# Optimization experiments

Measured on AMD Instinct MI355X. Metric: run time of the kernel, lower is better.

## Reference

```python
import jax, jax.numpy as jnp
import numpy as np

KS = 2        # kernel_size
DIL = 1       # dilation
FILTERS = 512
Z_DIM = 128
B, C, T = 8, 512, 4096
TZ = T + 2 * (KS - 1)


def _conv1d(x, w, b):
    # x: (B, L, Cin), w: (ks, Cin, Cout) -> VALID conv, channels-last (keras Conv1D)
    y = jax.lax.conv_general_dilated(x, w, window_strides=(1,), padding='VALID',
                                     dimension_numbers=('NWC', 'WIO', 'NWC'))
    return y + b


def _adaptor(z, w1, b1, w2, b2):
    return _conv1d(jax.nn.relu(_conv1d(z, w1, b1)), w2, b2)


def setup_inputs() -> dict:
    key = jax.random.key(0)
    ks = jax.random.split(key, 10)
    lim = np.sqrt(6.0 / FILTERS)
    u = lambda k, shp: jax.random.uniform(k, shp, jnp.float32, -lim, lim)
    return {
        'x': jax.random.normal(ks[0], (B, C, T), jnp.float32),
        'z': jax.random.normal(ks[1], (B, TZ, Z_DIM), jnp.float32),
        'ww1': u(ks[2], (KS, Z_DIM, FILTERS)), 'wb1': jnp.zeros((FILTERS,), jnp.float32),
        'ww2': u(ks[3], (KS, FILTERS, FILTERS)), 'wb2': jnp.zeros((FILTERS,), jnp.float32),
        'bw1': u(ks[4], (KS, Z_DIM, FILTERS)), 'bb1': jnp.zeros((FILTERS,), jnp.float32),
        'bw2': u(ks[5], (KS, FILTERS, FILTERS)), 'bb2': jnp.zeros((FILTERS,), jnp.float32),
    }


def reference(x, z, ww1, wb1, ww2, wb2, bw1, bb1, bw2, bb2):
    m = x.shape[1]
    t = x.shape[2]
    pad = DIL * (KS - 1)
    xp = jnp.pad(x, ((0, 0), (0, 0), (0, pad)))
    end = t + pad
    # im2col-style unfold: (B, C*KS, T)
    xu = jnp.concatenate([xp[:, :, pad - i * DIL: end - i * DIL] for i in range(KS)], axis=1)
    weights = _adaptor(z, ww1, wb1, ww2, wb2)   # (B, T, F)
    bias = _adaptor(z, bw1, bb1, bw2, bb2)      # (B, T, F)
    y = jnp.matmul(xu, weights)                 # (B, C*KS, F)
    return y[:, :m, :] + bias[:, :m, :]
```

## Files before the change

kernel.cpp:

```cpp
#include <hip/hip_runtime.h>

typedef short short8 __attribute__((ext_vector_type(8)));
typedef float float4v __attribute__((ext_vector_type(4)));
typedef __attribute__((address_space(1))) const unsigned int gu32;
typedef __attribute__((address_space(3))) unsigned int lu32;

__device__ __forceinline__ unsigned short f2bf(float f) {
  unsigned int u = __builtin_bit_cast(unsigned int, f);
  u += 0x7FFFu + ((u >> 16) & 1u);
  return (unsigned short)(u >> 16);
}
__device__ __forceinline__ float bf2f(unsigned short s) {
  return __builtin_bit_cast(float, (unsigned int)s << 16);
}

__global__ __launch_bounds__(256) void prep_w(
    const float* __restrict__ ww1, const float* __restrict__ ww2,
    const float* __restrict__ bw1, const float* __restrict__ bw2,
    const float* __restrict__ z,
    unsigned short* __restrict__ w1T, unsigned short* __restrict__ w2T,
    unsigned short* __restrict__ b1T, unsigned short* __restrict__ b2T,
    unsigned short* __restrict__ zb)
{
  int i = blockIdx.x * 256 + threadIdx.x;
  if (i < 131072) {
    int n = i & 511, k = i >> 9;
    w1T[n * 256 + k] = f2bf(ww1[i]);
  } else if (i < 655360) {
    int j = i - 131072; int n = j & 511, k = j >> 9;
    w2T[n * 1024 + k] = f2bf(ww2[j]);
  } else if (i < 786432) {
    int j = i - 655360; int n = j & 511, k = j >> 9;
    b1T[n * 256 + k] = f2bf(bw1[j]);
  } else if (i < 1310720) {
    int j = i - 786432; int n = j & 511, k = j >> 9;
    b2T[n * 1024 + k] = f2bf(bw2[j]);
  } else {
    int j = i - 1310720;
    zb[j] = f2bf(z[j]);
  }
}

template<int BM, int BN, bool RELU, bool OBF16, bool TRANS, bool SPLITK, int NH,
         bool ROWPACK, bool DBUF>
__device__ __forceinline__ void gemm_core(
    int bx, int by, int bz, int nzTot, unsigned short* smem,
    const unsigned short* __restrict__ A,
    const unsigned short* __restrict__ A2,
    const unsigned short* __restrict__ Bt,
    const float* __restrict__ biasv,
    void* __restrict__ outp,
    void* __restrict__ outp2,
    int M, int Kchunk, int RPB, int EXTRA, int BSCALE,
    int nHalf, int bRowMask,
    long long bStrideB, long long outBatchStride, int outLd)
{
  constexpr int WM = BM / 2, WN = BN / 2;
  constexpr int NI = WM / 16, NJ = WN / 16;
  constexpr int AI = BM / 64;
  constexpr int BI = BN / 64;
  constexpr int SA1 = BM * 32, SB1 = BN * 32;
  static_assert(!DBUF || (AI + BI == 4), "vmcnt immediates assume 4 glds/stage");
  unsigned short* sB0 = smem + NH * SA1;

  const int tid  = threadIdx.x;
  const int lane = tid & 63;
  const int wave = tid >> 6;
  const int wm = wave >> 1, wn = wave & 1;
  const int lr = lane & 15, quad = lane >> 4;

  const int r0 = bx * BM;
  const int n0 = by * BN;
  const int bb = r0 / RPB;
  const int Ktot = SPLITK ? Kchunk * nzTot : Kchunk;
  const int kOff = SPLITK ? bz * Kchunk : 0;
  const long long bOffB = (long long)bb * bStrideB;
  const unsigned short* Ae = (nHalf && n0 >= nHalf) ? A2 : A;

  const int srow = lane >> 2;
  const int sg = (lane & 3) ^ (srow & 3);
  const unsigned short* gA[AI];
#pragma unroll
  for (int c = 0; c < AI; ++c) {
    int instr = c * 4 + wave;
    int row = instr * 16 + srow;
    int r = r0 + row; if (r > M - 1) r = M - 1;
    gA[c] = Ae + ((long long)r + (long long)(r / RPB) * EXTRA) * BSCALE + kOff + sg * 8;
  }
  const unsigned short* gB[BI];
#pragma unroll
  for (int c = 0; c < BI; ++c) {
    int instr = c * 4 + wave;
    int row = instr * 16 + srow;
    gB[c] = Bt + (long long)((n0 + row) & bRowMask) * Ktot + bOffB + kOff + sg * 8;
  }

  int aoff[NI], boff[NJ];
#pragma unroll
  for (int i = 0; i < NI; ++i) {
    int rr = wm * WM + i * 16 + lr;
    aoff[i] = rr * 32 + ((quad ^ (rr & 3)) * 8);
  }
#pragma unroll
  for (int j = 0; j < NJ; ++j) {
    int rr = wn * WN + j * 16 + lr;
    boff[j] = rr * 32 + ((quad ^ (rr & 3)) * 8);
  }

  float4v acc[NI][NJ];
  const float4v z4 = {0.f, 0.f, 0.f, 0.f};
#pragma unroll
  for (int i = 0; i < NI; ++i)
#pragma unroll
    for (int j = 0; j < NJ; ++j) acc[i][j] = z4;

  if (DBUF) {
    constexpr int RS = SA1 + SB1;
    const int NT = Kchunk >> 5;
    auto stg = [&](int t, int m) {
      unsigned short* rb = smem + m * RS;
      int kk = t * 32;
#pragma unroll
      for (int c = 0; c < AI; ++c)
        __builtin_amdgcn_global_load_lds((gu32*)(gA[c] + kk),
                                         (lu32*)(rb + (c * 4 + wave) * 512), 16, 0, 0);
#pragma unroll
      for (int c = 0; c < BI; ++c)
        __builtin_amdgcn_global_load_lds((gu32*)(gB[c] + kk),
                                         (lu32*)(rb + SA1 + (c * 4 + wave) * 512), 16, 0, 0);
    };
    stg(0, 0); stg(1, 1);
    int m = 0;
    for (int t = 0; t < NT; ++t) {
      if (t + 1 < NT) asm volatile("s_waitcnt vmcnt(4)" ::: "memory");
      else            asm volatile("s_waitcnt vmcnt(0)" ::: "memory");
      __builtin_amdgcn_s_barrier();
      __builtin_amdgcn_sched_barrier(0);
      int m2 = m + 2; if (m2 >= 3) m2 -= 3;
      if (t + 2 < NT) stg(t + 2, m2);
      const unsigned short* rb = smem + m * RS;
      short8 af[NI], bfr[NJ];
#pragma unroll
      for (int i = 0; i < NI; ++i) af[i] = *(const short8*)(rb + aoff[i]);
#pragma unroll
      for (int j = 0; j < NJ; ++j) bfr[j] = *(const short8*)(rb + SA1 + boff[j]);
#pragma unroll
      for (int i = 0; i < NI; ++i)
#pragma unroll
        for (int j = 0; j < NJ; ++j)
          acc[i][j] = __builtin_amdgcn_mfma_f32_16x16x32_bf16(af[i], bfr[j], acc[i][j], 0, 0, 0);
      if (++m == 3) m = 0;
    }
    __syncthreads();
  } else {
    for (int k0 = 0; k0 < Kchunk; k0 += 32 * NH) {
#pragma unroll
      for (int h = 0; h < NH; ++h) {
#pragma unroll
        for (int c = 0; c < AI; ++c)
          __builtin_amdgcn_global_load_lds((gu32*)(gA[c] + k0 + h * 32),
                                           (lu32*)(smem + (c * 4 + wave) * 512 + h * SA1), 16, 0, 0);
#pragma unroll
        for (int c = 0; c < BI; ++c)
          __builtin_amdgcn_global_load_lds((gu32*)(gB[c] + k0 + h * 32),
                                           (lu32*)(sB0 + (c * 4 + wave) * 512 + h * SB1), 16, 0, 0);
      }
      __syncthreads();
#pragma unroll
      for (int h = 0; h < NH; ++h) {
        short8 af[NI], bfr[NJ];
#pragma unroll
        for (int i = 0; i < NI; ++i) af[i] = *(const short8*)(smem + h * SA1 + aoff[i]);
#pragma unroll
        for (int j = 0; j < NJ; ++j) bfr[j] = *(const short8*)(sB0 + h * SB1 + boff[j]);
#pragma unroll
        for (int i = 0; i < NI; ++i)
#pragma unroll
          for (int j = 0; j < NJ; ++j)
            acc[i][j] = __builtin_amdgcn_mfma_f32_16x16x32_bf16(af[i], bfr[j], acc[i][j], 0, 0, 0);
      }
      __syncthreads();
    }
  }

  if (TRANS) {
    unsigned short* Ts = smem;
    const int t0l = r0 - bb * RPB;
#pragma unroll
    for (int p = 0; p < 2; ++p) {
      if (wn == p) {
#pragma unroll
        for (int j = 0; j < NJ; ++j) {
          int frl = j * 16 + lr;
          float bv = biasv[n0 + p * WN + frl];
#pragma unroll
          for (int i = 0; i < NI; ++i) {
            int tr = wm * WM + i * 16 + quad * 4;
            unsigned long long pk = 0;
#pragma unroll
            for (int g = 0; g < 4; ++g) {
              float vv = acc[i][j][g] + bv;
              if (RELU) vv = fmaxf(vv, 0.f);
              pk |= (unsigned long long)f2bf(vv) << (16 * g);
            }
            *(unsigned long long*)(Ts + frl * (BM + 8) + tr) = pk;
          }
        }
      }
      __syncthreads();
      int frl = tid >> 2, sgg = tid & 3;
      unsigned short* dst = (unsigned short*)outp + (long long)bb * outBatchStride
                          + (long long)(n0 + p * WN + frl) * outLd + t0l + sgg * (BM / 4);
      const unsigned short* srcp = Ts + frl * (BM + 8) + sgg * (BM / 4);
#pragma unroll
      for (int u = 0; u < BM / 32; ++u)
        *(uint4*)(dst + u * 8) = *(const uint4*)(srcp + u * 8);
      __syncthreads();
    }
  } else if (ROWPACK) {
    constexpr int P  = (BM > 64) ? 2 : 1;
    constexpr int RP = BM / P;
    constexpr int BNP = BN + 8;
    constexpr int TPR = 256 / RP;
    constexpr int EPT = BN / TPR;
    void* op = (SPLITK && bz) ? outp2 : outp;
    unsigned short* R = smem;
#pragma unroll
    for (int p = 0; p < P; ++p) {
      if (P == 1 || wm == p) {
#pragma unroll
        for (int j = 0; j < NJ; ++j) {
          int cc = wn * WN + j * 16 + lr;
#pragma unroll
          for (int i = 0; i < NI; ++i) {
            int rl = (P == 1 ? wm * WM : 0) + i * 16 + quad * 4;
#pragma unroll
            for (int g = 0; g < 4; ++g)
              R[(rl + g) * BNP + cc] = f2bf(acc[i][j][g]);
          }
        }
      }
      __syncthreads();
      int rloc = tid / TPR, part = tid % TPR;
      unsigned short* dstp = (unsigned short*)op
                           + (long long)(r0 + p * RP + rloc) * outLd + n0 + part * EPT;
      const unsigned short* srcp = R + rloc * BNP + part * EPT;
#pragma unroll
      for (int u = 0; u < EPT / 8; ++u)
        *(uint4*)(dstp + u * 8) = *(const uint4*)(srcp + u * 8);
      if (p + 1 < P) __syncthreads();
    }
  } else {
    void* op = (SPLITK && bz) ? outp2 : outp;
#pragma unroll
    for (int j = 0; j < NJ; ++j) {
      int n_g = n0 + wn * WN + j * 16 + lr;
      float bv = biasv ? biasv[n_g] : 0.f;
#pragma unroll
      for (int i = 0; i < NI; ++i) {
        int r_base = r0 + wm * WM + i * 16 + quad * 4;
#pragma unroll
        for (int g = 0; g < 4; ++g) {
          int r_g = r_base + g;
          if (r_g >= M) continue;
          float v = acc[i][j][g] + bv;
          if (RELU) v = fmaxf(v, 0.f);
          long long oidx = (long long)r_g * outLd + n_g;
          if (OBF16) ((unsigned short*)op)[oidx] = f2bf(v);
          else       ((float*)op)[oidx] = v;
        }
      }
    }
  }
}

template<int BM, int BN, bool RELU, bool OBF16, bool TRANS, bool SPLITK, int NH,
         bool ROWPACK, bool DBUF, bool REMAP8>
__global__ __launch_bounds__(256)
void gemm_bt(const unsigned short* __restrict__ A,
             const unsigned short* __restrict__ A2,
             const unsigned short* __restrict__ Bt,
             const float* __restrict__ biasv,
             void* __restrict__ outp,
             void* __restrict__ outp2,
             int M, int Kchunk, int RPB, int EXTRA, int BSCALE,
             int nHalf, int bRowMask,
             long long bStrideB, long long outBatchStride, int outLd)
{
  constexpr int STAGE = DBUF ? 3 * (BM * 32 + BN * 32) : NH * (BM * 32 + BN * 32);
  constexpr int REPK = TRANS ? (BN / 2) * (BM + 8)
                     : (ROWPACK ? (BM > 64 ? (BM / 2) * (BN + 8) : BM * (BN + 8)) : 0);
  constexpr int SMEMN = (REPK > STAGE) ? REPK : STAGE;
  __shared__ unsigned short smem[SMEMN];
  int bx, by, bz, nz;
  if (REMAP8) {
    int lin = blockIdx.x;
    by = lin & 7;
    int pos = lin >> 3;
    bz = pos >> 5;
    bx = pos & 31;
    nz = 2;
  } else {
    bx = blockIdx.x; by = blockIdx.y; bz = blockIdx.z; nz = gridDim.z;
  }
  gemm_core<BM, BN, RELU, OBF16, TRANS, SPLITK, NH, ROWPACK, DBUF>(
      bx, by, bz, nz, smem,
      A, A2, Bt, biasv, outp, outp2,
      M, Kchunk, RPB, EXTRA, BSCALE, nHalf, bRowMask,
      bStrideB, outBatchStride, outLd);
}

__global__ __launch_bounds__(256) void mega(
    const float* __restrict__ x,
    const unsigned short* __restrict__ zb,
    const unsigned short* __restrict__ w1T,
    const unsigned short* __restrict__ b1T,
    const float* __restrict__ wb1,
    const float* __restrict__ bb1,
    unsigned short* __restrict__ h1T,
    unsigned short* __restrict__ h1b,
    unsigned short* __restrict__ xs,
    unsigned short* __restrict__ xz,
    float* __restrict__ rs)
{
  __shared__ unsigned short smem[8704];
  int b = blockIdx.x;
  int g = (b * 1284) / 5380;
  bool isg = (((b + 1) * 1284) / 5380) > g;
  if (isg) {
    if (g < 1024) {
      gemm_core<128, 128, true, true, true, false, 1, false, false>(
          g & 255, g >> 8, 0, 1, smem,
          zb, nullptr, w1T, wb1, h1T, nullptr,
          32768, 256, 4096, 2, 128, 0, 0xFFFF, 0, 512ll * 4096, 4096);
    } else {
      int idx = g - 1024;
      gemm_core<64, 128, true, true, false, false, 1, false, false>(
          idx % 65, idx / 65, 0, 1, smem,
          zb, nullptr, b1T, bb1, h1b, nullptr,
          4104, 256, 513, 3585, 128, 0, 0xFFFF, 0, 0, 512);
    }
  } else {
    float* red = (float*)smem;
    long long r = b - g;
    const float* xr = x + r * 4096;
    int t0 = threadIdx.x * 16;
    float v[17];
    const float4* xr4 = (const float4*)(xr + t0);
#pragma unroll
    for (int q = 0; q < 4; ++q) {
      float4 f = xr4[q];
      v[q * 4] = f.x; v[q * 4 + 1] = f.y; v[q * 4 + 2] = f.z; v[q * 4 + 3] = f.w;
    }
    v[16] = (t0 + 16 < 4096) ? xr[t0 + 16] : 0.f;
    unsigned int spk[8], zpk[8];
    float sum = 0.f;
#pragma unroll
    for (int q = 0; q < 8; ++q) {
      unsigned short s0 = f2bf(v[2 * q + 1]);
      unsigned short s1 = f2bf(v[2 * q + 2]);
      sum += bf2f(s0);
      sum += bf2f(s1);
      spk[q] = (unsigned int)s0 | ((unsigned int)s1 << 16);
      unsigned short z0 = (t0 == 0 && q == 0) ? (unsigned short)0 : f2bf(v[2 * q]);
      unsigned short z1 = f2bf(v[2 * q + 1]);
      zpk[q] = (unsigned int)z0 | ((unsigned int)z1 << 16);
    }
    *(uint4*)(xs + r * 4096 + t0)     = *(uint4*)(spk);
    *(uint4*)(xs + r * 4096 + t0 + 8) = *(uint4*)(spk + 4);
    *(uint4*)(xz + r * 4096 + t0)     = *(uint4*)(zpk);
    *(uint4*)(xz + r * 4096 + t0 + 8) = *(uint4*)(zpk + 4);
#pragma unroll
    for (int off = 32; off > 0; off >>= 1) sum += __shfl_down(sum, off);
    if ((threadIdx.x & 63) == 0) red[threadIdx.x >> 6] = sum;
    __syncthreads();
    if (threadIdx.x == 0) rs[r] = red[0] + red[1] + red[2] + red[3];
  }
}

__global__ __launch_bounds__(256) void final_gemm3(
    const unsigned short* __restrict__ p0,
    const unsigned short* __restrict__ p1,
    const unsigned short* __restrict__ h1b,
    const unsigned short* __restrict__ w2T,
    const unsigned short* __restrict__ b2T,
    const float* __restrict__ rs,
    const float* __restrict__ wb2,
    const float* __restrict__ bb2,
    float* __restrict__ out)
{
  constexpr int RS = 8192;
  __shared__ unsigned short smem[3 * RS];
  const int tid = threadIdx.x;
  const int lane = tid & 63, wave = tid >> 6;
  const int wm = wave >> 1, wn = wave & 1;
  const int lr = lane & 15, quad = lane >> 4;
  const int r0 = blockIdx.x * 64, n0 = blockIdx.y * 64;

  const int srow = lane >> 2;
  const int sg = (lane & 3) ^ (srow & 3);
  const int row = wave * 16 + srow;
  const int rA = r0 + row;
  const int rB = n0 + row;
  const unsigned short* aP[3] = {
    p0 + (long long)rA * 1024 + sg * 8,
    p1 + (long long)rA * 1024 + sg * 8,
    h1b + ((long long)rA + (rA >> 9)) * 512 + sg * 8 };
  const unsigned short* bP[3] = {
    w2T + (long long)rB * 1024 + sg * 8,
    w2T + (long long)rB * 1024 + sg * 8,
    b2T + (long long)rB * 1024 + sg * 8 };

  int aoff[2], boff[2];
#pragma unroll
  for (int i = 0; i < 2; ++i) {
    int rr = wm * 32 + i * 16 + lr;
    aoff[i] = rr * 32 + ((quad ^ (rr & 3)) * 8);
    int nn = wn * 32 + i * 16 + lr;
    boff[i] = nn * 32 + ((quad ^ (nn & 3)) * 8);
  }

  float4v acc[2][2];
  const float4v z4 = {0.f, 0.f, 0.f, 0.f};
  acc[0][0] = z4; acc[0][1] = z4; acc[1][0] = z4; acc[1][1] = z4;

  const int wslot = wave * 512;
  auto stg = [&](int t, int m) {
    int k = t * 64; int seg = k >> 10; int kk = k & 1023;
    unsigned short* base = smem + m * RS;
    __builtin_amdgcn_global_load_lds((gu32*)(aP[seg] + kk),      (lu32*)(base + wslot), 16, 0, 0);
    __builtin_amdgcn_global_load_lds((gu32*)(aP[seg] + kk + 32), (lu32*)(base + 2048 + wslot), 16, 0, 0);
    __builtin_amdgcn_global_load_lds((gu32*)(bP[seg] + kk),      (lu32*)(base + 4096 + wslot), 16, 0, 0);
    __builtin_amdgcn_global_load_lds((gu32*)(bP[seg] + kk + 32), (lu32*)(base + 6144 + wslot), 16, 0, 0);
  };
  stg(0, 0); stg(1, 1);
  int m = 0;
  for (int t = 0; t < 48; ++t) {
    if (t < 47) asm volatile("s_waitcnt vmcnt(4)" ::: "memory");
    else        asm volatile("s_waitcnt vmcnt(0)" ::: "memory");
    __builtin_amdgcn_s_barrier();
    __builtin_amdgcn_sched_barrier(0);
    int m2 = m + 2; if (m2 >= 3) m2 -= 3;
    if (t + 2 < 48) stg(t + 2, m2);
    const unsigned short* base = smem + m * RS;
#pragma unroll
    for (int h = 0; h < 2; ++h) {
      short8 af[2], bfr[2];
      af[0] = *(const short8*)(base + h * 2048 + aoff[0]);
      af[1] = *(const short8*)(base + h * 2048 + aoff[1]);
      bfr[0] = *(const short8*)(base + 4096 + h * 2048 + boff[0]);
      bfr[1] = *(const short8*)(base + 4096 + h * 2048 + boff[1]);
#pragma unroll
      for (int i = 0; i < 2; ++i)
#pragma unroll
        for (int j = 0; j < 2; ++j)
          acc[i][j] = __builtin_amdgcn_mfma_f32_16x16x32_bf16(af[i], bfr[j], acc[i][j], 0, 0, 0);
    }
    if (++m == 3) m = 0;
  }

#pragma unroll
  for (int j = 0; j < 2; ++j) {
    int n_g = n0 + wn * 32 + j * 16 + lr;
    float w2b = wb2[n_g], bbv = bb2[n_g];
#pragma unroll
    for (int i = 0; i < 2; ++i) {
      int rb2 = r0 + wm * 32 + i * 16 + quad * 4;
#pragma unroll
      for (int g = 0; g < 4; ++g) {
        int r_g = rb2 + g;
        out[(long long)r_g * 512 + n_g] = acc[i][j][g] + rs[r_g] * w2b + bbv;
      }
    }
  }
}

extern "C" void kernel_launch(void* const* d_in, const int* in_sizes, int n_in,
                              void* d_out, int out_size, void* d_ws, size_t ws_size,
                              hipStream_t stream) {
  const float* x   = (const float*)d_in[0];
  const float* z   = (const float*)d_in[1];
  const float* ww1 = (const float*)d_in[2];
  const float* wb1 = (const float*)d_in[3];
  const float* ww2 = (const float*)d_in[4];
  const float* wb2 = (const float*)d_in[5];
  const float* bw1 = (const float*)d_in[6];
  const float* bb1 = (const float*)d_in[7];
  const float* bw2 = (const float*)d_in[8];
  const float* bb2 = (const float*)d_in[9];

  char* ws = (char*)d_ws;
  unsigned short* xs  = (unsigned short*)ws; ws += 16777216ll * 2;
  unsigned short* xz  = (unsigned short*)ws; ws += 16777216ll * 2;
  unsigned short* zb  = (unsigned short*)ws; ws += 4196352ll  * 2;
  unsigned short* h1T = (unsigned short*)ws; ws += 16777216ll * 2;
  unsigned short* h1b = (unsigned short*)ws; ws += 2101248ll  * 2;
  unsigned short* w2T = (unsigned short*)ws; ws += 524288ll * 2;
  unsigned short* b2T = (unsigned short*)ws; ws += 524288ll * 2;
  float* rs = (float*)ws;                    ws += 4096ll * 4;
  char* tail = ws;
  unsigned short* w1T = (unsigned short*)tail;
  unsigned short* b1T = (unsigned short*)tail + 131072;
  unsigned short* p0  = zb;
  unsigned short* p1  = (unsigned short*)tail;

  prep_w<<<21512, 256, 0, stream>>>(ww1, ww2, bw1, bw2, z, w1T, w2T, b1T, b2T, zb);
  mega<<<5380, 256, 0, stream>>>(x, zb, w1T, b1T, wb1, bb1, h1T, h1b, xs, xz, rs);
  gemm_bt<128, 128, false, true, false, true, 1, true, true, true><<<512, 256, 0, stream>>>(
      xs, xz, h1T, nullptr, p0, p1,
      4096, 2048, 512, 0, 4096, 512, 511, 512ll * 4096, 0, 1024);
  final_gemm3<<<dim3(64, 8), 256, 0, stream>>>(
      p0, p1, h1b, w2T, b2T, rs, wb2, bb2, (float*)d_out);
}
```

Baseline: 248.6 us.

## Split fused mega kernel into x conversion and pipelined conv1 GEMM kernels

The interleaved mega kernel, which mixed the x-to-bf16 conversion blocks with the first adaptor-conv GEMM blocks, is split into two launches: cvt_x and conv1. The conv1 GEMMs now use the triple-buffered global_load_lds pipeline (DBUF) with a larger shared-memory allocation, and the vmcnt wait count is made generic over loads per stage. This trades the overlap of memory-bound conversion with compute-bound GEMM for a better-pipelined GEMM loop, at the cost of an extra launch and higher LDS use per block, which may lower occupancy.

```diff
diff --git a/kernel.cpp b/kernel.cpp
--- a/kernel.cpp
+++ b/kernel.cpp
@@ -12,6 +12,15 @@
 }
 __device__ __forceinline__ float bf2f(unsigned short s) {
   return __builtin_bit_cast(float, (unsigned int)s << 16);
+}
+
+template<int N> __device__ __forceinline__ void vmwait() {
+  if constexpr (N == 0) asm volatile("s_waitcnt vmcnt(0)" ::: "memory");
+  else if constexpr (N == 2) asm volatile("s_waitcnt vmcnt(2)" ::: "memory");
+  else if constexpr (N == 3) asm volatile("s_waitcnt vmcnt(3)" ::: "memory");
+  else if constexpr (N == 4) asm volatile("s_waitcnt vmcnt(4)" ::: "memory");
+  else if constexpr (N == 6) asm volatile("s_waitcnt vmcnt(6)" ::: "memory");
+  else if constexpr (N == 8) asm volatile("s_waitcnt vmcnt(8)" ::: "memory");
 }
 
 __global__ __launch_bounds__(256) void prep_w(
@@ -60,7 +69,6 @@
   constexpr int AI = BM / 64;
   constexpr int BI = BN / 64;
   constexpr int SA1 = BM * 32, SB1 = BN * 32;
-  static_assert(!DBUF || (AI + BI == 4), "vmcnt immediates assume 4 glds/stage");
   unsigned short* sB0 = smem + NH * SA1;
 
   const int tid  = threadIdx.x;
@@ -132,8 +140,8 @@
     stg(0, 0); stg(1, 1);
     int m = 0;
     for (int t = 0; t < NT; ++t) {
-      if (t + 1 < NT) asm volatile("s_waitcnt vmcnt(4)" ::: "memory");
-      else            asm volatile("s_waitcnt vmcnt(0)" ::: "memory");
+      if (t + 1 < NT) vmwait<AI + BI>();
+      else            vmwait<0>();
       __builtin_amdgcn_s_barrier();
       __builtin_amdgcn_sched_barrier(0);
       int m2 = m + 2; if (m2 >= 3) m2 -= 3;
@@ -310,71 +318,70 @@
       bStrideB, outBatchStride, outLd);
 }
 
-__global__ __launch_bounds__(256) void mega(
+__global__ __launch_bounds__(256) void cvt_x(
     const float* __restrict__ x,
+    unsigned short* __restrict__ xs,
+    unsigned short* __restrict__ xz,
+    float* __restrict__ rs)
+{
+  __shared__ float red[4];
+  long long r = blockIdx.x;
+  const float* xr = x + r * 4096;
+  int t0 = threadIdx.x * 16;
+  float v[17];
+  const float4* xr4 = (const float4*)(xr + t0);
+#pragma unroll
+  for (int q = 0; q < 4; ++q) {
+    float4 f = xr4[q];
+    v[q * 4] = f.x; v[q * 4 + 1] = f.y; v[q * 4 + 2] = f.z; v[q * 4 + 3] = f.w;
+  }
+  v[16] = (t0 + 16 < 4096) ? xr[t0 + 16] : 0.f;
+  unsigned int spk[8], zpk[8];
+  float sum = 0.f;
+#pragma unroll
+  for (int q = 0; q < 8; ++q) {
+    unsigned short s0 = f2bf(v[2 * q + 1]);
+    unsigned short s1 = f2bf(v[2 * q + 2]);
+    sum += bf2f(s0);
+    sum += bf2f(s1);
+    spk[q] = (unsigned int)s0 | ((unsigned int)s1 << 16);
+    unsigned short z0 = (t0 == 0 && q == 0) ? (unsigned short)0 : f2bf(v[2 * q]);
+    unsigned short z1 = f2bf(v[2 * q + 1]);
+    zpk[q] = (unsigned int)z0 | ((unsigned int)z1 << 16);
+  }
+  *(uint4*)(xs + r * 4096 + t0)     = *(uint4*)(spk);
+  *(uint4*)(xs + r * 4096 + t0 + 8) = *(uint4*)(spk + 4);
+  *(uint4*)(xz + r * 4096 + t0)     = *(uint4*)(zpk);
+  *(uint4*)(xz + r * 4096 + t0 + 8) = *(uint4*)(zpk + 4);
+#pragma unroll
+  for (int off = 32; off > 0; off >>= 1) sum += __shfl_down(sum, off);
+  if ((threadIdx.x & 63) == 0) red[threadIdx.x >> 6] = sum;
+  __syncthreads();
+  if (threadIdx.x == 0) rs[r] = red[0] + red[1] + red[2] + red[3];
+}
+
+__global__ __launch_bounds__(256) void conv1(
     const unsigned short* __restrict__ zb,
     const unsigned short* __restrict__ w1T,
     const unsigned short* __restrict__ b1T,
     const float* __restrict__ wb1,
     const float* __restrict__ bb1,
     unsigned short* __restrict__ h1T,
-    unsigned short* __restrict__ h1b,
-    unsigned short* __restrict__ xs,
-    unsigned short* __restrict__ xz,
-    float* __restrict__ rs)
+    unsigned short* __restrict__ h1b)
 {
-  __shared__ unsigned short smem[8704];
-  int b = blockIdx.x;
-  int g = (b * 1284) / 5380;
-  bool isg = (((b + 1) * 1284) / 5380) > g;
-  if (isg) {
-    if (g < 1024) {
-      gemm_core<128, 128, true, true, true, false, 1, false, false>(
-          g & 255, g >> 8, 0, 1, smem,
-          zb, nullptr, w1T, wb1, h1T, nullptr,
-          32768, 256, 4096, 2, 128, 0, 0xFFFF, 0, 512ll * 4096, 4096);
-    } else {
-      int idx = g - 1024;
-      gemm_core<64, 128, true, true, false, false, 1, false, false>(
-          idx % 65, idx / 65, 0, 1, smem,
-          zb, nullptr, b1T, bb1, h1b, nullptr,
-          4104, 256, 513, 3585, 128, 0, 0xFFFF, 0, 0, 512);
-    }
+  __shared__ unsigned short smem[24576];
+  int g = blockIdx.x;
+  if (g < 1024) {
+    gemm_core<128, 128, true, true, true, false, 1, false, true>(
+        g & 255, g >> 8, 0, 1, smem,
+        zb, nullptr, w1T, wb1, h1T, nullptr,
+        32768, 256, 4096, 2, 128, 0, 0xFFFF, 0, 512ll * 4096, 4096);
   } else {
-    float* red = (float*)smem;
-    long long r = b - g;
-    const float* xr = x + r * 4096;
-    int t0 = threadIdx.x * 16;
-    float v[17];
-    const float4* xr4 = (const float4*)(xr + t0);
-#pragma unroll
-    for (int q = 0; q < 4; ++q) {
-      float4 f = xr4[q];
-      v[q * 4] = f.x; v[q * 4 + 1] = f.y; v[q * 4 + 2] = f.z; v[q * 4 + 3] = f.w;
-    }
-    v[16] = (t0 + 16 < 4096) ? xr[t0 + 16] : 0.f;
-    unsigned int spk[8], zpk[8];
-    float sum = 0.f;
-#pragma unroll
-    for (int q = 0; q < 8; ++q) {
-      unsigned short s0 = f2bf(v[2 * q + 1]);
-      unsigned short s1 = f2bf(v[2 * q + 2]);
-      sum += bf2f(s0);
-      sum += bf2f(s1);
-      spk[q] = (unsigned int)s0 | ((unsigned int)s1 << 16);
-      unsigned short z0 = (t0 == 0 && q == 0) ? (unsigned short)0 : f2bf(v[2 * q]);
-      unsigned short z1 = f2bf(v[2 * q + 1]);
-      zpk[q] = (unsigned int)z0 | ((unsigned int)z1 << 16);
-    }
-    *(uint4*)(xs + r * 4096 + t0)     = *(uint4*)(spk);
-    *(uint4*)(xs + r * 4096 + t0 + 8) = *(uint4*)(spk + 4);
-    *(uint4*)(xz + r * 4096 + t0)     = *(uint4*)(zpk);
-    *(uint4*)(xz + r * 4096 + t0 + 8) = *(uint4*)(zpk + 4);
-#pragma unroll
-    for (int off = 32; off > 0; off >>= 1) sum += __shfl_down(sum, off);
-    if ((threadIdx.x & 63) == 0) red[threadIdx.x >> 6] = sum;
-    __syncthreads();
-    if (threadIdx.x == 0) rs[r] = red[0] + red[1] + red[2] + red[3];
+    int idx = g - 1024;
+    gemm_core<64, 128, true, true, false, false, 1, false, true>(
+        idx % 65, idx / 65, 0, 1, smem,
+        zb, nullptr, b1T, bb1, h1b, nullptr,
+        4104, 256, 513, 3585, 128, 0, 0xFFFF, 0, 0, 512);
   }
 }
 
@@ -436,8 +443,8 @@
   stg(0, 0); stg(1, 1);
   int m = 0;
   for (int t = 0; t < 48; ++t) {
-    if (t < 47) asm volatile("s_waitcnt vmcnt(4)" ::: "memory");
-    else        asm volatile("s_waitcnt vmcnt(0)" ::: "memory");
+    if (t < 47) vmwait<4>();
+    else        vmwait<0>();
     __builtin_amdgcn_s_barrier();
     __builtin_amdgcn_sched_barrier(0);
     int m2 = m + 2; if (m2 >= 3) m2 -= 3;
@@ -505,7 +512,8 @@
   unsigned short* p1  = (unsigned short*)tail;
 
   prep_w<<<21512, 256, 0, stream>>>(ww1, ww2, bw1, bw2, z, w1T, w2T, b1T, b2T, zb);
-  mega<<<5380, 256, 0, stream>>>(x, zb, w1T, b1T, wb1, bb1, h1T, h1b, xs, xz, rs);
+  cvt_x<<<4096, 256, 0, stream>>>(x, xs, xz, rs);
+  conv1<<<1284, 256, 0, stream>>>(zb, w1T, b1T, wb1, bb1, h1T, h1b);
   gemm_bt<128, 128, false, true, false, true, 1, true, true, true><<<512, 256, 0, stream>>>(
       xs, xz, h1T, nullptr, p0, p1,
       4096, 2048, 512, 0, 4096, 512, 511, 512ll * 4096, 0, 1024);
```

Result: no change. 250.7 us (+0.8%).
